# Kernel optimization log

Hardware: AMD Instinct MI355X
Metric: run time of the kernel (lower is better)

## Reference

```python
import jax, jax.numpy as jnp
import numpy as np

GRADIENT_MUL = 0.1


def _base_offset(k):
    # matches torch module: y repeated, x tiled, interleaved (y,x) pairs -> [2*k*k]
    pad = (k - 1) // 2
    r = np.arange(-pad, pad + 1, dtype=np.float32)
    by = np.repeat(r, k)
    bx = np.tile(r, k)
    return np.stack([by, bx], axis=1).reshape(-1)


def _deform_conv(feat, offset, weight, k):
    # feat: [B,C,H,W], offset: [B,2*k*k,H,W] (y,x interleaved), weight: [Co,C,k,k]
    B, C, H, W = feat.shape
    pad = (k - 1) // 2
    KK = k * k
    off = offset.reshape(B, KK, 2, H, W)
    r = jnp.arange(k, dtype=feat.dtype) - pad
    gy = jnp.repeat(r, k)[None, :, None, None]          # kernel grid y per tap
    gx = jnp.tile(r, (k,))[None, :, None, None]         # kernel grid x per tap
    ys = jnp.arange(H, dtype=feat.dtype)[None, None, :, None] + gy + off[:, :, 0]  # [B,KK,H,W]
    xs = jnp.arange(W, dtype=feat.dtype)[None, None, None, :] + gx + off[:, :, 1]
    feat_flat = feat.reshape(B, C, H * W)
    y0 = jnp.floor(ys)
    x0 = jnp.floor(xs)
    dy = ys - y0
    dx = xs - x0
    val = jnp.zeros((B, C, KK * H * W), feat.dtype)
    # bilinear sample with zero padding outside bounds (4 corners)
    for yy, wy in ((y0, 1.0 - dy), (y0 + 1.0, dy)):
        for xx, wx in ((x0, 1.0 - dx), (x0 + 1.0, dx)):
            valid = (yy >= 0) & (yy < H) & (xx >= 0) & (xx < W)
            yi = jnp.clip(yy, 0, H - 1).astype(jnp.int32)
            xi = jnp.clip(xx, 0, W - 1).astype(jnp.int32)
            idx = (yi * W + xi).reshape(B, -1)                   # [B, KK*H*W]
            g = jax.vmap(lambda f, i: f[:, i])(feat_flat, idx)   # [B, C, KK*H*W]
            w = (wy * wx * valid.astype(feat.dtype)).reshape(B, 1, -1)
            val = val + g * w
    sampled = val.reshape(B, C, KK, H, W)
    wmat = weight.reshape(weight.shape[0], C, KK)
    return jnp.einsum('bckhw,ock->bohw', sampled, wmat)


def setup_inputs() -> dict:
    key = jax.random.key(0)
    k1, k2, k3, k4, k5 = jax.random.split(key, 5)
    B, C, H, W = 2, 256, 64, 64
    feat = jax.random.normal(k1, (B, C, H, W), dtype=jnp.float32)
    deform_offset = jax.random.normal(k2, (B, 2 * (9 + 25 + 49), H, W), dtype=jnp.float32)
    w3 = jax.random.normal(k3, (256, C, 3, 3), dtype=jnp.float32) * 0.01
    w5 = jax.random.normal(k4, (256, C, 5, 5), dtype=jnp.float32) * 0.01
    w7 = jax.random.normal(k5, (256, C, 7, 7), dtype=jnp.float32) * 0.01
    return {"feat": feat, "deform_offset": deform_offset, "w3": w3, "w5": w5, "w7": w7}


def reference(feat, deform_offset, w3, w5, w7):
    outs = []
    start = 0
    for k, w in ((3, w3), (5, w5), (7, w7)):
        n = 2 * k * k
        off = deform_offset[:, start:start + n]
        start += n
        # gradient-mul trick: value unchanged, gradient scaled by GRADIENT_MUL
        off = GRADIENT_MUL * off + (1.0 - GRADIENT_MUL) * jax.lax.stop_gradient(off)
        base = jnp.asarray(_base_offset(k), dtype=feat.dtype)[None, :, None, None]
        outs.append(_deform_conv(feat, off - base, w, k))
    return jnp.concatenate(outs, axis=1)
```

## Files before the change

kernel.cpp:

```cpp
#include <hip/hip_runtime.h>

using bf16x8 = __attribute__((ext_vector_type(8))) short;
using f32x4  = __attribute__((ext_vector_type(4))) float;

#define HW   4096
#define CIN  256
#define OFFC 166

#define WS3_BASE 0
#define WS5_BASE 589824
#define WS7_BASE 2228224
#define WS_TOTAL 5439488
#define WBYTES   (WS_TOTAL * 2)
#define QELEMS   1048576
#define QBYTES   (QELEMS * 16)

__device__ __forceinline__ unsigned short f2bf(float f) {
    unsigned u = __builtin_bit_cast(unsigned, f);
    return (unsigned short)((u + 0x7fffu + ((u >> 16) & 1u)) >> 16);
}
__device__ __forceinline__ float bf2f(unsigned v) {
    return __builtin_bit_cast(float, v << 16);
}
__device__ __forceinline__ unsigned cvt_pk_bf16(float lo, float hi) {
    unsigned r;
    asm volatile("v_cvt_pk_bf16_f32 %0, %1, %2" : "=v"(r) : "v"(lo), "v"(hi));
    return r;
}

__global__ __launch_bounds__(256)
void mcdc_prep_w(const float* __restrict__ w3, const float* __restrict__ w5,
                 const float* __restrict__ w7, unsigned short* __restrict__ ws)
{
    int idx = blockIdx.x * 256 + threadIdx.x;
    const float* src; int KKv, base;
    if (idx < WS5_BASE)      { src = w3; KKv = 9;  base = WS3_BASE; }
    else if (idx < WS7_BASE) { src = w5; KKv = 25; base = WS5_BASE; }
    else                     { src = w7; KKv = 49; base = WS7_BASE; }
    int rel = idx - base;
    int e  = rel & 7;
    int l  = (rel >> 3) & 63;
    int gm = (rel >> 9) & 15;
    int ks = rel >> 13;
    int o  = gm * 16 + (l & 15);
    int r  = ks * 32 + (l >> 4) * 8 + e;
    ws[idx] = f2bf(src[((size_t)o * CIN + (r & 255)) * KKv + (r >> 8)]);
}

__global__ __launch_bounds__(256)
void mcdc_prep_q(const float* __restrict__ feat, uint4* __restrict__ q)
{
    int idx = blockIdx.x * 256 + threadIdx.x;
    int b = idx >> 19, c2 = (idx >> 12) & 127, pos = idx & 4095;
    int y = pos >> 6, x = pos & 63;
    int xp = min(x + 1, 63), yp = min(y + 1, 63);
    const float* f0 = feat + ((size_t)(b * CIN + 2 * c2)) * HW;
    const float* f1 = f0 + HW;
    uint4 o;
    o.x = (unsigned)f2bf(f0[y  * 64 + x]) | ((unsigned)f2bf(f0[y  * 64 + xp]) << 16);
    o.y = (unsigned)f2bf(f0[yp * 64 + x]) | ((unsigned)f2bf(f0[yp * 64 + xp]) << 16);
    o.z = (unsigned)f2bf(f1[y  * 64 + x]) | ((unsigned)f2bf(f1[y  * 64 + xp]) << 16);
    o.w = (unsigned)f2bf(f1[yp * 64 + x]) | ((unsigned)f2bf(f1[yp * 64 + xp]) << 16);
    q[idx] = o;
}

template<int K, int CH_OFF, int OC_OFF, bool ATOMIC, int MODE>
__device__ __forceinline__ void dconv(
    const float* __restrict__ feat, const float* __restrict__ off,
    const unsigned short* __restrict__ wsA, const uint4* __restrict__ qf,
    float* __restrict__ out, int b, int p0, int ks0, int ks1,
    unsigned short (&sB)[2][64][40])
{
    const int tid  = threadIdx.x;
    const int lane = tid & 63;
    const int wid  = tid >> 6;
    const int mh   = wid & 1;
    const int pq   = wid >> 1;
    const int pxs  = tid & 63;
    const int coct = wid;

    const int pix = p0 + pxs, py = pix >> 6, px = pix & 63;

    const uint4* qbase[2];
    const float* fbase[2];
    int   fxo[2], fyo[2];
    float mw[2][4];

    auto computeMeta = [&](int j) {
        const int s = j & 1;
        const float* ob = off + ((size_t)(b * OFFC + CH_OFF + 2 * j)) * HW + pix;
        const float oy = ob[0], ox = ob[HW];
        const float sy = (float)py + oy, sx = (float)px + ox;
        const float fy = floorf(sy), fx = floorf(sx);
        const float dy = sy - fy, dx = sx - fx;
        const int y0 = (int)fy, x0 = (int)fx;
        const bool vy0 = (y0 >= 0) & (y0 < 64), vy1 = (y0 >= -1) & (y0 < 63);
        const bool vx0 = (x0 >= 0) & (x0 < 64), vx1 = (x0 >= -1) & (x0 < 63);
        float w00 = (1.f - dy) * (1.f - dx) * ((vy0 && vx0) ? 1.f : 0.f);
        float w01 = (1.f - dy) * dx         * ((vy0 && vx1) ? 1.f : 0.f);
        float w10 = dy * (1.f - dx)         * ((vy1 && vx0) ? 1.f : 0.f);
        float w11 = dy * dx                 * ((vy1 && vx1) ? 1.f : 0.f);
        const int ya  = min(max(y0, 0), 63),     xa  = min(max(x0, 0), 63);
        const int y1c = min(max(y0 + 1, 0), 63), x1c = min(max(x0 + 1, 0), 63);
        if (x1c == xa) { w00 += w01; w10 += w11; w01 = 0.f; w11 = 0.f; }
        if (y1c == ya) { w00 += w10; w01 += w11; w10 = 0.f; w11 = 0.f; }
        mw[s][0] = w00; mw[s][1] = w01; mw[s][2] = w10; mw[s][3] = w11;
        const int base = ya * 64 + xa;
        if (MODE == 0) {
            qbase[s] = qf + (((size_t)(b * 128 + coct * 2)) << 12) + base;
        } else {
            fbase[s] = feat + ((size_t)(b * CIN)) * HW + base;
            fxo[s] = x1c - xa; fyo[s] = (y1c - ya) * 64;
        }
    };

    uint4 gA0, gA1, gB0, gB1;
    float fA[16], fB[16];

    auto gissue = [&](int ks, uint4& g0, uint4& g1, float* f) {
        const int s = (ks >> 3) & 1;
        if (MODE == 0) {
            const uint4* qp = qbase[s] + ((ks & 7) << 16);
            g0 = qp[0];
            g1 = qp[4096];
        } else {
            const float* fp = fbase[s] + ((size_t)((ks & 7) * 32 + coct * 4)) * HW;
            const int xo = fxo[s], yo = fyo[s];
#pragma unroll
            for (int e = 0; e < 4; ++e) {
                f[e*4+0] = fp[0]; f[e*4+1] = fp[xo]; f[e*4+2] = fp[yo]; f[e*4+3] = fp[yo+xo];
                fp += HW;
            }
        }
    };

    auto bwrite = [&](int ks, const uint4& g0, const uint4& g1, const float* f) {
        const int s = (ks >> 3) & 1;
        const float w00 = mw[s][0], w01 = mw[s][1], w10 = mw[s][2], w11 = mw[s][3];
        float v[4];
        if (MODE == 0) {
            v[0] = w00*bf2f(g0.x & 0xffff) + w01*bf2f(g0.x >> 16)
                 + w10*bf2f(g0.y & 0xffff) + w11*bf2f(g0.y >> 16);
            v[1] = w00*bf2f(g0.z & 0xffff) + w01*bf2f(g0.z >> 16)
                 + w10*bf2f(g0.w & 0xffff) + w11*bf2f(g0.w >> 16);
            v[2] = w00*bf2f(g1.x & 0xffff) + w01*bf2f(g1.x >> 16)
                 + w10*bf2f(g1.y & 0xffff) + w11*bf2f(g1.y >> 16);
            v[3] = w00*bf2f(g1.z & 0xffff) + w01*bf2f(g1.z >> 16)
                 + w10*bf2f(g1.w & 0xffff) + w11*bf2f(g1.w >> 16);
        } else {
#pragma unroll
            for (int e = 0; e < 4; ++e)
                v[e] = w00*f[e*4] + w01*f[e*4+1] + w10*f[e*4+2] + w11*f[e*4+3];
        }
        uint2 wv;
        wv.x = cvt_pk_bf16(v[0], v[1]);
        wv.y = cvt_pk_bf16(v[2], v[3]);
        *(uint2*)(&sB[ks & 1][pxs][coct * 4]) = wv;
    };

    f32x4 acc[8];
#pragma unroll
    for (int i = 0; i < 8; ++i) acc[i] = f32x4{0.f, 0.f, 0.f, 0.f};

    auto iter = [&](int ks, uint4& gc0, uint4& gc1, float* fc,
                    uint4& gn0, uint4& gn1, float* fn) {
        __syncthreads();
        if ((ks & 7) == 6 && ks + 2 < ks1) computeMeta((ks + 2) >> 3);
        { const int kg = min(ks + 2, ks1 - 1); gissue(kg, gn0, gn1, fn); }
        const bf16x8 bfr = *(const bf16x8*)(&sB[ks & 1][pq * 16 + (lane & 15)][(lane >> 4) * 8]);
        const unsigned short* ap = wsA + (((size_t)ks * 16 + mh * 8) * 64 + lane) * 8;
        bf16x8 a[8];
#pragma unroll
        for (int mf = 0; mf < 8; ++mf) a[mf] = *(const bf16x8*)(ap + mf * 512);
        if (ks + 1 < ks1) bwrite(ks + 1, gc0, gc1, fc);
#pragma unroll
        for (int mf = 0; mf < 8; ++mf)
            acc[mf] = __builtin_amdgcn_mfma_f32_16x16x32_bf16(a[mf], bfr, acc[mf], 0, 0, 0);
    };

    computeMeta(ks0 >> 3);
    gissue(ks0, gA0, gA1, fA);
    gissue(min(ks0 + 1, ks1 - 1), gB0, gB1, fB);
    bwrite(ks0, gA0, gA1, fA);

    for (int ks = ks0; ks < ks1; ks += 2) {
        iter(ks,     gB0, gB1, fB, gA0, gA1, fA);
        iter(ks + 1, gA0, gA1, fA, gB0, gB1, fB);
    }

#pragma unroll
    for (int mf = 0; mf < 8; ++mf) {
#pragma unroll
        for (int r = 0; r < 4; ++r) {
            const int o = OC_OFF + mh * 128 + mf * 16 + (lane >> 4) * 4 + r;
            const int p = p0 + pq * 16 + (lane & 15);
            float* dst = out + ((size_t)(b * 768 + o)) * HW + p;
            if (ATOMIC) atomicAdd(dst, acc[mf][r]);
            else        *dst = acc[mf][r];
        }
    }
}

template<int MODE>
__global__ __launch_bounds__(512, 4)
void mcdc_main(const float* __restrict__ feat, const float* __restrict__ off,
               const unsigned short* __restrict__ ws, const uint4* __restrict__ qf,
               float* __restrict__ out)
{
    __shared__ __attribute__((aligned(16))) unsigned short sB[2][64][40];

    const int bid  = blockIdx.x;
    const int xcd  = bid & 7;
    const int tl   = (bid >> 3) & 15;
    const int role = bid >> 7;
    const int tile = xcd * 16 + tl;
    const int b    = tile >> 6;
    const int p0   = (tile & 63) << 6;

    if (role == 0) {
        dconv<3, 0, 0, false, MODE>(feat, off, ws + WS3_BASE, qf, out, b, p0, 0, 72, sB);
    } else if (role <= 7) {
        const int r = role - 1;
        dconv<7, 68, 512, true, MODE>(feat, off, ws + WS7_BASE, qf, out, b, p0,
                                      r * 56, r * 56 + 56, sB);
    } else {
        const int r = role - 8;
        const int ks0 = r * 48;
        const int ks1 = (r == 3) ? 200 : ks0 + 48;
        dconv<5, 18, 256, true, MODE>(feat, off, ws + WS5_BASE, qf, out, b, p0,
                                      ks0, ks1, sB);
    }
}

extern "C" void kernel_launch(void* const* d_in, const int* in_sizes, int n_in,
                              void* d_out, int out_size, void* d_ws, size_t ws_size,
                              hipStream_t stream)
{
    const float* feat = (const float*)d_in[0];
    const float* off  = (const float*)d_in[1];
    const float* w3   = (const float*)d_in[2];
    const float* w5   = (const float*)d_in[3];
    const float* w7   = (const float*)d_in[4];
    float* out = (float*)d_out;
    unsigned short* ws = (unsigned short*)d_ws;
    uint4* qf = (uint4*)((char*)d_ws + WBYTES);

    hipMemsetAsync(d_out, 0, (size_t)out_size * sizeof(float), stream);
    mcdc_prep_w<<<dim3(WS_TOTAL / 256), dim3(256), 0, stream>>>(w3, w5, w7, ws);

    if (ws_size >= (size_t)WBYTES + QBYTES) {
        mcdc_prep_q<<<dim3(QELEMS / 256), dim3(256), 0, stream>>>(feat, qf);
        mcdc_main<0><<<dim3(1536), dim3(512), 0, stream>>>(feat, off, ws, qf, out);
    } else {
        mcdc_main<2><<<dim3(1536), dim3(512), 0, stream>>>(feat, off, ws, nullptr, out);
    }
}
```

Measured before the change: 374.8 us.

## Process two K-steps per barrier with four-stage shared B buffer

```diff
diff --git a/kernel.cpp b/kernel.cpp
--- a/kernel.cpp
+++ b/kernel.cpp
@@ -69,7 +69,7 @@
     const float* __restrict__ feat, const float* __restrict__ off,
     const unsigned short* __restrict__ wsA, const uint4* __restrict__ qf,
     float* __restrict__ out, int b, int p0, int ks0, int ks1,
-    unsigned short (&sB)[2][64][40])
+    unsigned short (&sB)[4][64][40])
 {
     const int tid  = threadIdx.x;
     const int lane = tid & 63;
@@ -114,8 +114,8 @@
         }
     };
 
-    uint4 gA0, gA1, gB0, gB1;
-    float fA[16], fB[16];
+    uint4 A0g0, A0g1, A1g0, A1g1, B0g0, B0g1, B1g0, B1g1;
+    float fA0[16], fA1[16], fB0[16], fB1[16];
 
     auto gissue = [&](int ks, uint4& g0, uint4& g1, float* f) {
         const int s = (ks >> 3) & 1;
@@ -155,37 +155,59 @@
         uint2 wv;
         wv.x = cvt_pk_bf16(v[0], v[1]);
         wv.y = cvt_pk_bf16(v[2], v[3]);
-        *(uint2*)(&sB[ks & 1][pxs][coct * 4]) = wv;
+        *(uint2*)(&sB[ks & 3][pxs][coct * 4]) = wv;
     };
 
     f32x4 acc[8];
 #pragma unroll
     for (int i = 0; i < 8; ++i) acc[i] = f32x4{0.f, 0.f, 0.f, 0.f};
 
-    auto iter = [&](int ks, uint4& gc0, uint4& gc1, float* fc,
-                    uint4& gn0, uint4& gn1, float* fn) {
+    auto pairIter = [&](int ks,
+                        uint4& c0g0, uint4& c0g1, float* cf0,
+                        uint4& c1g0, uint4& c1g1, float* cf1,
+                        uint4& n0g0, uint4& n0g1, float* nf0,
+                        uint4& n1g0, uint4& n1g1, float* nf1) {
         __syncthreads();
-        if ((ks & 7) == 6 && ks + 2 < ks1) computeMeta((ks + 2) >> 3);
-        { const int kg = min(ks + 2, ks1 - 1); gissue(kg, gn0, gn1, fn); }
-        const bf16x8 bfr = *(const bf16x8*)(&sB[ks & 1][pq * 16 + (lane & 15)][(lane >> 4) * 8]);
-        const unsigned short* ap = wsA + (((size_t)ks * 16 + mh * 8) * 64 + lane) * 8;
-        bf16x8 a[8];
-#pragma unroll
-        for (int mf = 0; mf < 8; ++mf) a[mf] = *(const bf16x8*)(ap + mf * 512);
-        if (ks + 1 < ks1) bwrite(ks + 1, gc0, gc1, fc);
-#pragma unroll
-        for (int mf = 0; mf < 8; ++mf)
-            acc[mf] = __builtin_amdgcn_mfma_f32_16x16x32_bf16(a[mf], bfr, acc[mf], 0, 0, 0);
+        if ((ks & 7) == 4 && ks + 4 < ks1) computeMeta((ks + 4) >> 3);
+        { const int kg = min(ks + 4, ks1 - 1); gissue(kg, n0g0, n0g1, nf0); }
+        { const int kg = min(ks + 5, ks1 - 1); gissue(kg, n1g0, n1g1, nf1); }
+        const bf16x8 bfr0 = *(const bf16x8*)(&sB[ks & 3][pq * 16 + (lane & 15)][(lane >> 4) * 8]);
+        const bf16x8 bfr1 = *(const bf16x8*)(&sB[(ks + 1) & 3][pq * 16 + (lane & 15)][(lane >> 4) * 8]);
+        {
+            const unsigned short* ap = wsA + (((size_t)ks * 16 + mh * 8) * 64 + lane) * 8;
+            bf16x8 a[8];
+#pragma unroll
+            for (int mf = 0; mf < 8; ++mf) a[mf] = *(const bf16x8*)(ap + mf * 512);
+            if (ks + 2 < ks1) bwrite(ks + 2, c0g0, c0g1, cf0);
+#pragma unroll
+            for (int mf = 0; mf < 8; ++mf)
+                acc[mf] = __builtin_amdgcn_mfma_f32_16x16x32_bf16(a[mf], bfr0, acc[mf], 0, 0, 0);
+        }
+        {
+            const unsigned short* ap = wsA + (((size_t)(ks + 1) * 16 + mh * 8) * 64 + lane) * 8;
+            bf16x8 a[8];
+#pragma unroll
+            for (int mf = 0; mf < 8; ++mf) a[mf] = *(const bf16x8*)(ap + mf * 512);
+            if (ks + 2 < ks1) bwrite(ks + 3, c1g0, c1g1, cf1);
+#pragma unroll
+            for (int mf = 0; mf < 8; ++mf)
+                acc[mf] = __builtin_amdgcn_mfma_f32_16x16x32_bf16(a[mf], bfr1, acc[mf], 0, 0, 0);
+        }
     };
 
     computeMeta(ks0 >> 3);
-    gissue(ks0, gA0, gA1, fA);
-    gissue(min(ks0 + 1, ks1 - 1), gB0, gB1, fB);
-    bwrite(ks0, gA0, gA1, fA);
-
-    for (int ks = ks0; ks < ks1; ks += 2) {
-        iter(ks,     gB0, gB1, fB, gA0, gA1, fA);
-        iter(ks + 1, gA0, gA1, fA, gB0, gB1, fB);
+    gissue(ks0,     A0g0, A0g1, fA0);
+    gissue(ks0 + 1, A1g0, A1g1, fA1);
+    bwrite(ks0,     A0g0, A0g1, fA0);
+    bwrite(ks0 + 1, A1g0, A1g1, fA1);
+    gissue(ks0 + 2, B0g0, B0g1, fB0);
+    gissue(ks0 + 3, B1g0, B1g1, fB1);
+
+    for (int ks = ks0; ks < ks1; ks += 4) {
+        pairIter(ks,     B0g0, B0g1, fB0, B1g0, B1g1, fB1,
+                         A0g0, A0g1, fA0, A1g0, A1g1, fA1);
+        pairIter(ks + 2, A0g0, A0g1, fA0, A1g0, A1g1, fA1,
+                         B0g0, B0g1, fB0, B1g0, B1g1, fB1);
     }
 
 #pragma unroll
@@ -207,7 +229,7 @@
                const unsigned short* __restrict__ ws, const uint4* __restrict__ qf,
                float* __restrict__ out)
 {
-    __shared__ __attribute__((aligned(16))) unsigned short sB[2][64][40];
+    __shared__ __attribute__((aligned(16))) unsigned short sB[4][64][40];
 
     const int bid  = blockIdx.x;
     const int xcd  = bid & 7;
```

Measured after the change: 401.8 us. 1.07x slower.

## Stage weight tiles through double-buffered LDS instead of direct global loads

Applied to the files above, without the earlier changes.

```diff
diff --git a/kernel.cpp b/kernel.cpp
--- a/kernel.cpp
+++ b/kernel.cpp
@@ -69,7 +69,7 @@
     const float* __restrict__ feat, const float* __restrict__ off,
     const unsigned short* __restrict__ wsA, const uint4* __restrict__ qf,
     float* __restrict__ out, int b, int p0, int ks0, int ks1,
-    unsigned short (&sB)[2][64][40])
+    unsigned short (&sB)[2][64][40], unsigned short (&sA)[2][8192])
 {
     const int tid  = threadIdx.x;
     const int lane = tid & 63;
@@ -116,6 +116,7 @@
 
     uint4 gA0, gA1, gB0, gB1;
     float fA[16], fB[16];
+    uint4 aP0, aP1, aQ0, aQ1;
 
     auto gissue = [&](int ks, uint4& g0, uint4& g1, float* f) {
         const int s = (ks >> 3) & 1;
@@ -132,6 +133,17 @@
                 fp += HW;
             }
         }
+    };
+
+    auto gissueA = [&](int ks, uint4& h0, uint4& h1) {
+        const uint4* src = (const uint4*)(wsA + (size_t)ks * 8192) + tid * 2;
+        h0 = src[0];
+        h1 = src[1];
+    };
+    auto awrite = [&](int ks, const uint4& h0, const uint4& h1) {
+        uint4* dst = (uint4*)(&sA[ks & 1][tid * 16]);
+        dst[0] = h0;
+        dst[1] = h1;
     };
 
     auto bwrite = [&](int ks, const uint4& g0, const uint4& g1, const float* f) {
@@ -163,16 +175,20 @@
     for (int i = 0; i < 8; ++i) acc[i] = f32x4{0.f, 0.f, 0.f, 0.f};
 
     auto iter = [&](int ks, uint4& gc0, uint4& gc1, float* fc,
-                    uint4& gn0, uint4& gn1, float* fn) {
+                    uint4& gn0, uint4& gn1, float* fn,
+                    uint4& wc0, uint4& wc1, uint4& wn0, uint4& wn1) {
         __syncthreads();
         if ((ks & 7) == 6 && ks + 2 < ks1) computeMeta((ks + 2) >> 3);
-        { const int kg = min(ks + 2, ks1 - 1); gissue(kg, gn0, gn1, fn); }
+        { const int kg = min(ks + 2, ks1 - 1); gissue(kg, gn0, gn1, fn); gissueA(kg, wn0, wn1); }
         const bf16x8 bfr = *(const bf16x8*)(&sB[ks & 1][pq * 16 + (lane & 15)][(lane >> 4) * 8]);
-        const unsigned short* ap = wsA + (((size_t)ks * 16 + mh * 8) * 64 + lane) * 8;
         bf16x8 a[8];
 #pragma unroll
-        for (int mf = 0; mf < 8; ++mf) a[mf] = *(const bf16x8*)(ap + mf * 512);
-        if (ks + 1 < ks1) bwrite(ks + 1, gc0, gc1, fc);
+        for (int mf = 0; mf < 8; ++mf)
+            a[mf] = *(const bf16x8*)(&sA[ks & 1][(mh * 8 + mf) * 512 + lane * 8]);
+        if (ks + 1 < ks1) {
+            bwrite(ks + 1, gc0, gc1, fc);
+            awrite(ks + 1, wc0, wc1);
+        }
 #pragma unroll
         for (int mf = 0; mf < 8; ++mf)
             acc[mf] = __builtin_amdgcn_mfma_f32_16x16x32_bf16(a[mf], bfr, acc[mf], 0, 0, 0);
@@ -180,12 +196,15 @@
 
     computeMeta(ks0 >> 3);
     gissue(ks0, gA0, gA1, fA);
+    gissueA(ks0, aP0, aP1);
     gissue(min(ks0 + 1, ks1 - 1), gB0, gB1, fB);
+    gissueA(min(ks0 + 1, ks1 - 1), aQ0, aQ1);
     bwrite(ks0, gA0, gA1, fA);
+    awrite(ks0, aP0, aP1);
 
     for (int ks = ks0; ks < ks1; ks += 2) {
-        iter(ks,     gB0, gB1, fB, gA0, gA1, fA);
-        iter(ks + 1, gA0, gA1, fA, gB0, gB1, fB);
+        iter(ks,     gB0, gB1, fB, gA0, gA1, fA, aQ0, aQ1, aP0, aP1);
+        iter(ks + 1, gA0, gA1, fA, gB0, gB1, fB, aP0, aP1, aQ0, aQ1);
     }
 
 #pragma unroll
@@ -208,6 +227,7 @@
                float* __restrict__ out)
 {
     __shared__ __attribute__((aligned(16))) unsigned short sB[2][64][40];
+    __shared__ __attribute__((aligned(16))) unsigned short sA[2][8192];
 
     const int bid  = blockIdx.x;
     const int xcd  = bid & 7;
@@ -218,17 +238,17 @@
     const int p0   = (tile & 63) << 6;
 
     if (role == 0) {
-        dconv<3, 0, 0, false, MODE>(feat, off, ws + WS3_BASE, qf, out, b, p0, 0, 72, sB);
+        dconv<3, 0, 0, false, MODE>(feat, off, ws + WS3_BASE, qf, out, b, p0, 0, 72, sB, sA);
     } else if (role <= 7) {
         const int r = role - 1;
         dconv<7, 68, 512, true, MODE>(feat, off, ws + WS7_BASE, qf, out, b, p0,
-                                      r * 56, r * 56 + 56, sB);
+                                      r * 56, r * 56 + 56, sB, sA);
     } else {
         const int r = role - 8;
         const int ks0 = r * 48;
         const int ks1 = (r == 3) ? 200 : ks0 + 48;
         dconv<5, 18, 256, true, MODE>(feat, off, ws + WS5_BASE, qf, out, b, p0,
-                                      ks0, ks1, sB);
+                                      ks0, ks1, sB, sA);
     }
 }
 
```

Result: faster. 320.2 us (-14.6%).
